# Kernel tuning notes

Measured on AMD Instinct MI355X. Metric: run time of the kernel, lower is better.

## Reference

```python
import jax, jax.numpy as jnp
import numpy as np
from itertools import product

_EPS = 1e-5
N_VOX = 120000
C = 64
B, D, H, Wd = 2, 400, 400, 40  # batch and spatial voxel grid


def _build_rulebook(seed=0):
    """Random unique active voxels + [N,27] submanifold neighbor index table (-1 = inactive)."""
    rng = np.random.default_rng(seed)
    size = B * D * H * Wd
    flat = rng.choice(size, size=N_VOX, replace=False)
    b = flat // (D * H * Wd)
    rem = flat % (D * H * Wd)
    z = rem // (H * Wd)
    rem2 = rem % (H * Wd)
    y = rem2 // Wd
    x = rem2 % Wd
    lut = np.full(size, -1, np.int32)
    lut[flat] = np.arange(N_VOX, dtype=np.int32)
    offs = np.array(list(product([-1, 0, 1], repeat=3)), dtype=np.int64)  # [27,3]
    zz = z[:, None] + offs[None, :, 0]
    yy = y[:, None] + offs[None, :, 1]
    xx = x[:, None] + offs[None, :, 2]
    valid = (zz >= 0) & (zz < D) & (yy >= 0) & (yy < H) & (xx >= 0) & (xx < Wd)
    nf = ((b[:, None] * D + zz) * H + yy) * Wd + xx
    nbr = np.where(valid, lut[np.clip(nf, 0, size - 1)], -1).astype(np.int32)
    return nbr


def setup_inputs() -> dict:
    key = jax.random.key(0)
    ks = jax.random.split(key, 12)
    nbr = jnp.asarray(_build_rulebook())
    return {
        "features": jax.random.normal(ks[0], (N_VOX, C), jnp.float32),
        "W1": jax.random.normal(ks[1], (27, C, C), jnp.float32) * 0.05,
        "g1": jax.random.uniform(ks[2], (C,), jnp.float32, 0.5, 1.5),
        "b1": jax.random.normal(ks[3], (C,), jnp.float32) * 0.1,
        "m1": jax.random.normal(ks[4], (C,), jnp.float32) * 0.1,
        "v1": jax.random.uniform(ks[5], (C,), jnp.float32, 0.5, 1.5),
        "W2": jax.random.normal(ks[6], (27, C, C), jnp.float32) * 0.05,
        "g2": jax.random.uniform(ks[7], (C,), jnp.float32, 0.5, 1.5),
        "b2": jax.random.normal(ks[8], (C,), jnp.float32) * 0.1,
        "m2": jax.random.normal(ks[9], (C,), jnp.float32) * 0.1,
        "v2": jax.random.uniform(ks[10], (C,), jnp.float32, 0.5, 1.5),
        "nbr_idx": nbr,
    }


def _subm_conv(f, nbr, W):
    # gather-GEMM: f [N,Cin], nbr [N,27], W [27,Cin,Cout] -> [N,Cout]
    mask = (nbr >= 0)[:, :, None]
    g = jnp.where(mask, f[jnp.clip(nbr, 0)], jnp.zeros((), f.dtype))  # [N,27,Cin]
    return jnp.einsum('nkc,kcd->nd', g, W)


def _bn(x, g, b, m, v):
    return (x - m) * (g * jax.lax.rsqrt(v + _EPS)) + b


def reference(features, W1, g1, b1, m1, v1, W2, g2, b2, m2, v2, nbr_idx):
    out = _bn(_subm_conv(features, nbr_idx, W1), g1, b1, m1, v1)
    out = jax.nn.relu(out)
    out = _bn(_subm_conv(out, nbr_idx, W2), g2, b2, m2, v2)
    return jax.nn.relu(out + features)
```

## Files before the change

kernel.cpp:

```cpp
#include <hip/hip_runtime.h>

typedef short short8 __attribute__((ext_vector_type(8)));
typedef float f32x4 __attribute__((ext_vector_type(4)));

#define N_VOX 120000
#define C64 64
#define K27 27
#define KC 13
#define TILES 3750
#define CAPT 64
#define LAYER_W 110592
#define CSRB 938
#define PACKB 65
#define FUSEB 938

#define WS_TCNT 0
#define WS_BNP  16384
#define WS_PWC  20480
#define WS_PWT  40960
#define WS_ENTS 524288
#define WS_MIDB (4u << 20)

__device__ __forceinline__ ushort f2bf(float x) {
    uint u = __float_as_uint(x);
    u = (u + 0x7FFFu + ((u >> 16) & 1u)) >> 16;
    return (ushort)u;
}
__device__ __forceinline__ float bf2f(ushort u) {
    return __uint_as_float((uint)u << 16);
}

__global__ __launch_bounds__(256) void prep_csr_kernel(
    const int* __restrict__ nbr,
    const float* __restrict__ W1, const float* __restrict__ W2,
    const float* g1, const float* b1, const float* m1, const float* v1,
    const float* g2, const float* b2, const float* m2, const float* v2,
    int* __restrict__ tcnt, int2* __restrict__ ents,
    ushort* __restrict__ pwt, ushort* __restrict__ pwc,
    float* __restrict__ bnp) {
    if (blockIdx.x < CSRB) {
        __shared__ int cnt_[4];
        const int wv = threadIdx.x >> 6, lane = threadIdx.x & 63;
        const int tile = blockIdx.x * 4 + wv;
        const bool act = tile < TILES;
        if (lane == 0) cnt_[wv] = 0;
        __syncthreads();
        if (act) {
            const int base = tile * (32 * K27);
            for (int e = lane; e < 32 * K27; e += 64) {
                const int k = e % K27;
                if (k == KC) continue;
                const int m = nbr[base + e];
                if (m >= 0) {
                    const int nl = e / K27;
                    int slot = atomicAdd(&cnt_[wv], 1);
                    if (slot < CAPT) ents[tile * CAPT + slot] = make_int2(nl | (k << 8), m);
                }
            }
        }
        __syncthreads();
        if (act && lane == 0) {
            int c = cnt_[wv];
            tcnt[tile] = c > CAPT ? CAPT : c;
        }
    } else {
        int idx = (blockIdx.x - CSRB) * 256 + threadIdx.x;
        const int stride = PACKB * 256;
        for (; idx < 229440; idx += stride) {
            if (idx < 221184) {
                int L = idx / LAYER_W, r = idx % LAYER_W;
                int k = r >> 12, dc = r & 4095, d = dc >> 6, c = dc & 63;
                const float* W = L ? W2 : W1;
                pwt[idx] = f2bf(W[(size_t)k * 4096 + c * 64 + d]);
            } else if (idx < 229376) {
                int j2 = idx - 221184;
                int L = j2 >> 12, q = j2 & 4095;
                int ks = q >> 11, tq = (q >> 9) & 3, ln = (q >> 3) & 63, jj = q & 7;
                int c = ks * 32 + (ln >> 4) * 8 + jj;
                int d = tq * 16 + (ln & 15);
                const float* W = L ? W2 : W1;
                pwc[L * 4096 + q] = f2bf(W[(size_t)KC * 4096 + c * 64 + d]);
            } else {
                int i = idx - 229376;
                float s1 = g1[i] * rsqrtf(v1[i] + 1e-5f);
                bnp[i] = s1; bnp[64 + i] = b1[i] - m1[i] * s1;
                float s2 = g2[i] * rsqrtf(v2[i] + 1e-5f);
                bnp[128 + i] = s2; bnp[192 + i] = b2[i] - m2[i] * s2;
            }
        }
    }
}

template <bool L2P>
__device__ __forceinline__ void fused_core(const float* __restrict__ f,
                                           const ushort* __restrict__ midin,
                                           const ushort* __restrict__ pwc,
                                           const ushort* __restrict__ pwt,
                                           const int* __restrict__ tcnt,
                                           const int2* __restrict__ ents,
                                           const float* __restrict__ bnp,
                                           ushort* __restrict__ midout,
                                           float* __restrict__ fout,
                                           float* exw, int tile) {
    const int lane = threadIdx.x & 63;
    const int r16 = lane & 15, kg = lane >> 4;
    const int n0 = tile * 32;

#pragma unroll
    for (int i = 0; i < 8; ++i) ((f32x4*)exw)[i * 64 + lane] = (f32x4)0.f;

    const short8* B = (const short8*)pwc;
    short8 Bf[2][4];
#pragma unroll
    for (int s = 0; s < 2; ++s)
#pragma unroll
        for (int t = 0; t < 4; ++t) Bf[s][t] = B[(s * 4 + t) * 64 + lane];

    f32x4 acc[2][4];
#pragma unroll
    for (int v = 0; v < 2; ++v)
#pragma unroll
        for (int t = 0; t < 4; ++t) acc[v][t] = (f32x4)0.f;

#pragma unroll
    for (int v = 0; v < 2; ++v) {
        short8 a0, a1;
        if (L2P) {
            const short8* ar = (const short8*)(midin + (size_t)(n0 + v * 16 + r16) * C64);
            a0 = ar[kg];
            a1 = ar[4 + kg];
        } else {
            const float4* ar = (const float4*)(f + (size_t)(n0 + v * 16 + r16) * C64);
            float4 fa = ar[kg * 2], fb = ar[kg * 2 + 1];
            float4 fc = ar[8 + kg * 2], fd = ar[9 + kg * 2];
            a0[0] = f2bf(fa.x); a0[1] = f2bf(fa.y); a0[2] = f2bf(fa.z); a0[3] = f2bf(fa.w);
            a0[4] = f2bf(fb.x); a0[5] = f2bf(fb.y); a0[6] = f2bf(fb.z); a0[7] = f2bf(fb.w);
            a1[0] = f2bf(fc.x); a1[1] = f2bf(fc.y); a1[2] = f2bf(fc.z); a1[3] = f2bf(fc.w);
            a1[4] = f2bf(fd.x); a1[5] = f2bf(fd.y); a1[6] = f2bf(fd.z); a1[7] = f2bf(fd.w);
        }
#pragma unroll
        for (int t = 0; t < 4; ++t) {
            acc[v][t] = __builtin_amdgcn_mfma_f32_16x16x32_bf16(a0, Bf[0][t], acc[v][t], 0, 0, 0);
            acc[v][t] = __builtin_amdgcn_mfma_f32_16x16x32_bf16(a1, Bf[1][t], acc[v][t], 0, 0, 0);
        }
    }

    const int cnt = tcnt[tile];
    for (int p = 0; p < cnt; ++p) {
        int2 e = ents[tile * CAPT + p];
        const int ex = __builtin_amdgcn_readfirstlane(e.x);
        const int m  = __builtin_amdgcn_readfirstlane(e.y);
        const int nl = ex & 255, k = ex >> 8;
        const short8* wr = (const short8*)(pwt + (size_t)k * 4096 + lane * 64);
        float ee0 = 0.f, ee1 = 0.f, ee2 = 0.f, ee3 = 0.f;
        if (L2P) {
            const uint* am = (const uint*)(midin + (size_t)m * C64);
#pragma unroll
            for (int g = 0; g < 8; ++g) {
                short8 w8 = wr[g];
                uint u0 = am[g * 4 + 0], u1 = am[g * 4 + 1];
                uint u2 = am[g * 4 + 2], u3 = am[g * 4 + 3];
                ee0 = fmaf(bf2f((ushort)u0),         bf2f((ushort)w8[0]), ee0);
                ee1 = fmaf(bf2f((ushort)(u0 >> 16)), bf2f((ushort)w8[1]), ee1);
                ee2 = fmaf(bf2f((ushort)u1),         bf2f((ushort)w8[2]), ee2);
                ee3 = fmaf(bf2f((ushort)(u1 >> 16)), bf2f((ushort)w8[3]), ee3);
                ee0 = fmaf(bf2f((ushort)u2),         bf2f((ushort)w8[4]), ee0);
                ee1 = fmaf(bf2f((ushort)(u2 >> 16)), bf2f((ushort)w8[5]), ee1);
                ee2 = fmaf(bf2f((ushort)u3),         bf2f((ushort)w8[6]), ee2);
                ee3 = fmaf(bf2f((ushort)(u3 >> 16)), bf2f((ushort)w8[7]), ee3);
            }
        } else {
            const float4* am = (const float4*)(f + (size_t)m * C64);
#pragma unroll
            for (int g = 0; g < 8; ++g) {
                short8 w8 = wr[g];
                float4 x0 = am[g * 2], x1 = am[g * 2 + 1];
                ee0 = fmaf(x0.x, bf2f((ushort)w8[0]), ee0);
                ee1 = fmaf(x0.y, bf2f((ushort)w8[1]), ee1);
                ee2 = fmaf(x0.z, bf2f((ushort)w8[2]), ee2);
                ee3 = fmaf(x0.w, bf2f((ushort)w8[3]), ee3);
                ee0 = fmaf(x1.x, bf2f((ushort)w8[4]), ee0);
                ee1 = fmaf(x1.y, bf2f((ushort)w8[5]), ee1);
                ee2 = fmaf(x1.z, bf2f((ushort)w8[6]), ee2);
                ee3 = fmaf(x1.w, bf2f((ushort)w8[7]), ee3);
            }
        }
        exw[nl * C64 + lane] += (ee0 + ee1) + (ee2 + ee3);
    }

#pragma unroll
    for (int v = 0; v < 2; ++v)
#pragma unroll
        for (int t = 0; t < 4; ++t)
#pragma unroll
            for (int r = 0; r < 4; ++r)
                exw[(v * 16 + kg * 4 + r) * C64 + t * 16 + r16] += acc[v][t][r];

    const int row = lane >> 1, col0 = (lane & 1) * 32;
    const f32x4* xl = (const f32x4*)(exw + row * C64 + col0);
    const size_t gbase = (size_t)(n0 + row) * C64 + col0;
    if (L2P) {
#pragma unroll
        for (int i = 0; i < 8; ++i) {
            f32x4 x = xl[i];
            float4 s  = *(const float4*)(bnp + col0 + i * 4);
            float4 h  = *(const float4*)(bnp + 64 + col0 + i * 4);
            float4 r4 = *(const float4*)(f + gbase + i * 4);
            float4 o;
            o.x = fmaxf(fmaf(x[0], s.x, h.x) + r4.x, 0.f);
            o.y = fmaxf(fmaf(x[1], s.y, h.y) + r4.y, 0.f);
            o.z = fmaxf(fmaf(x[2], s.z, h.z) + r4.z, 0.f);
            o.w = fmaxf(fmaf(x[3], s.w, h.w) + r4.w, 0.f);
            *(float4*)(fout + gbase + i * 4) = o;
        }
    } else {
#pragma unroll
        for (int i = 0; i < 4; ++i) {
            f32x4 x0 = xl[i * 2], x1 = xl[i * 2 + 1];
            float4 s0 = *(const float4*)(bnp + col0 + i * 8);
            float4 s1 = *(const float4*)(bnp + col0 + i * 8 + 4);
            float4 h0 = *(const float4*)(bnp + 64 + col0 + i * 8);
            float4 h1 = *(const float4*)(bnp + 64 + col0 + i * 8 + 4);
            short8 o;
            o[0] = f2bf(fmaxf(fmaf(x0[0], s0.x, h0.x), 0.f));
            o[1] = f2bf(fmaxf(fmaf(x0[1], s0.y, h0.y), 0.f));
            o[2] = f2bf(fmaxf(fmaf(x0[2], s0.z, h0.z), 0.f));
            o[3] = f2bf(fmaxf(fmaf(x0[3], s0.w, h0.w), 0.f));
            o[4] = f2bf(fmaxf(fmaf(x1[0], s1.x, h1.x), 0.f));
            o[5] = f2bf(fmaxf(fmaf(x1[1], s1.y, h1.y), 0.f));
            o[6] = f2bf(fmaxf(fmaf(x1[2], s1.z, h1.z), 0.f));
            o[7] = f2bf(fmaxf(fmaf(x1[3], s1.w, h1.w), 0.f));
            *(short8*)(midout + gbase + i * 8) = o;
        }
    }
}

__global__ __launch_bounds__(256) void fused_l1_kernel(const float* __restrict__ f,
                                                       const ushort* __restrict__ pwc,
                                                       const ushort* __restrict__ pwt,
                                                       const int* __restrict__ tcnt,
                                                       const int2* __restrict__ ents,
                                                       const float* __restrict__ bnp,
                                                       ushort* __restrict__ midb) {
    __shared__ float ext[4][32 * C64];
    const int wv = threadIdx.x >> 6;
    const int tile = blockIdx.x * 4 + wv;
    if (tile >= TILES) return;
    fused_core<false>(f, nullptr, pwc, pwt, tcnt, ents, bnp, midb, nullptr, ext[wv], tile);
}

__global__ __launch_bounds__(256) void fused_l2_kernel(const float* __restrict__ f,
                                                       const ushort* __restrict__ midb,
                                                       const ushort* __restrict__ pwc,
                                                       const ushort* __restrict__ pwt,
                                                       const int* __restrict__ tcnt,
                                                       const int2* __restrict__ ents,
                                                       const float* __restrict__ bnp,
                                                       float* __restrict__ out) {
    __shared__ float ext[4][32 * C64];
    const int wv = threadIdx.x >> 6;
    const int tile = blockIdx.x * 4 + wv;
    if (tile >= TILES) return;
    fused_core<true>(f, midb, pwc, pwt, tcnt, ents, bnp, nullptr, out, ext[wv], tile);
}

extern "C" void kernel_launch(void* const* d_in, const int* in_sizes, int n_in,
                              void* d_out, int out_size, void* d_ws, size_t ws_size,
                              hipStream_t stream) {
    const float* f   = (const float*)d_in[0];
    const float* W1  = (const float*)d_in[1];
    const float* g1  = (const float*)d_in[2];
    const float* b1  = (const float*)d_in[3];
    const float* m1  = (const float*)d_in[4];
    const float* v1  = (const float*)d_in[5];
    const float* W2  = (const float*)d_in[6];
    const float* g2  = (const float*)d_in[7];
    const float* b2  = (const float*)d_in[8];
    const float* m2  = (const float*)d_in[9];
    const float* v2  = (const float*)d_in[10];
    const int*   nbr = (const int*)d_in[11];
    float* out = (float*)d_out;

    char* ws = (char*)d_ws;
    int*    tcnt = (int*)(ws + WS_TCNT);
    float*  bnp  = (float*)(ws + WS_BNP);
    ushort* pwc  = (ushort*)(ws + WS_PWC);
    ushort* pwt  = (ushort*)(ws + WS_PWT);
    int2*   ents = (int2*)(ws + WS_ENTS);
    ushort* midb = (ushort*)(ws + WS_MIDB);

    prep_csr_kernel<<<CSRB + PACKB, 256, 0, stream>>>(
        nbr, W1, W2, g1, b1, m1, v1, g2, b2, m2, v2, tcnt, ents, pwt, pwc, bnp);

    fused_l1_kernel<<<FUSEB, 256, 0, stream>>>(f, pwc, pwt, tcnt, ents, bnp, midb);
    fused_l2_kernel<<<FUSEB, 256, 0, stream>>>(f, midb, pwc + 4096, pwt + LAYER_W,
                                               tcnt, ents, bnp + 128, out);
}
```

Baseline: 205.4 us.

## Shrink voxel tiles to 16 rows and stage neighbor entries in LDS

Halves the per-wave tile from 32 to 16 voxels, doubling the number of waves so more of them are resident, and cuts per-wave LDS use. The tile's neighbor-entry list is copied once into shared memory, and the pair loop is unrolled by two. LDS rows get padding to avoid bank conflicts, and the weight-pack stage becomes one element per thread. The trade-off is a smaller centre-tap MFMA per wave and a lower CAPT of 48, which raises the chance of silently dropping neighbor pairs in dense tiles.

```diff
diff --git a/kernel.cpp b/kernel.cpp
--- a/kernel.cpp
+++ b/kernel.cpp
@@ -7,17 +7,18 @@
 #define C64 64
 #define K27 27
 #define KC 13
-#define TILES 3750
-#define CAPT 64
+#define TIL 7500
+#define CAPT 48
+#define PAD 68
 #define LAYER_W 110592
-#define CSRB 938
-#define PACKB 65
-#define FUSEB 938
+#define CSRB 1875
+#define PACKB 897
+#define FUSEB 1875
 
 #define WS_TCNT 0
-#define WS_BNP  16384
-#define WS_PWC  20480
-#define WS_PWT  40960
+#define WS_BNP  32768
+#define WS_PWC  36864
+#define WS_PWT  65536
 #define WS_ENTS 524288
 #define WS_MIDB (4u << 20)
 
@@ -42,53 +43,93 @@
         __shared__ int cnt_[4];
         const int wv = threadIdx.x >> 6, lane = threadIdx.x & 63;
         const int tile = blockIdx.x * 4 + wv;
-        const bool act = tile < TILES;
         if (lane == 0) cnt_[wv] = 0;
         __syncthreads();
-        if (act) {
-            const int base = tile * (32 * K27);
-            for (int e = lane; e < 32 * K27; e += 64) {
-                const int k = e % K27;
-                if (k == KC) continue;
-                const int m = nbr[base + e];
-                if (m >= 0) {
-                    const int nl = e / K27;
-                    int slot = atomicAdd(&cnt_[wv], 1);
-                    if (slot < CAPT) ents[tile * CAPT + slot] = make_int2(nl | (k << 8), m);
-                }
+        const int base = tile * (16 * K27);
+#pragma unroll
+        for (int e = lane; e < 16 * K27; e += 64) {
+            const int k = e % K27;
+            if (k == KC) continue;
+            const int m = nbr[base + e];
+            if (m >= 0) {
+                const int nl = e / K27;
+                int slot = atomicAdd(&cnt_[wv], 1);
+                if (slot < CAPT) ents[tile * CAPT + slot] = make_int2(nl | (k << 8), m);
             }
         }
         __syncthreads();
-        if (act && lane == 0) {
+        if (lane == 0) {
             int c = cnt_[wv];
             tcnt[tile] = c > CAPT ? CAPT : c;
         }
     } else {
-        int idx = (blockIdx.x - CSRB) * 256 + threadIdx.x;
-        const int stride = PACKB * 256;
-        for (; idx < 229440; idx += stride) {
-            if (idx < 221184) {
-                int L = idx / LAYER_W, r = idx % LAYER_W;
-                int k = r >> 12, dc = r & 4095, d = dc >> 6, c = dc & 63;
-                const float* W = L ? W2 : W1;
-                pwt[idx] = f2bf(W[(size_t)k * 4096 + c * 64 + d]);
-            } else if (idx < 229376) {
-                int j2 = idx - 221184;
-                int L = j2 >> 12, q = j2 & 4095;
-                int ks = q >> 11, tq = (q >> 9) & 3, ln = (q >> 3) & 63, jj = q & 7;
-                int c = ks * 32 + (ln >> 4) * 8 + jj;
-                int d = tq * 16 + (ln & 15);
-                const float* W = L ? W2 : W1;
-                pwc[L * 4096 + q] = f2bf(W[(size_t)KC * 4096 + c * 64 + d]);
-            } else {
-                int i = idx - 229376;
-                float s1 = g1[i] * rsqrtf(v1[i] + 1e-5f);
-                bnp[i] = s1; bnp[64 + i] = b1[i] - m1[i] * s1;
-                float s2 = g2[i] * rsqrtf(v2[i] + 1e-5f);
-                bnp[128 + i] = s2; bnp[192 + i] = b2[i] - m2[i] * s2;
-            }
-        }
-    }
+        const int idx = (blockIdx.x - CSRB) * 256 + threadIdx.x;
+        if (idx < 221184) {
+            int L = idx / LAYER_W, r = idx % LAYER_W;
+            int k = r >> 12, dc = r & 4095, d = dc >> 6, c = dc & 63;
+            const float* W = L ? W2 : W1;
+            pwt[idx] = f2bf(W[(size_t)k * 4096 + c * 64 + d]);
+        } else if (idx < 229376) {
+            int j2 = idx - 221184;
+            int L = j2 >> 12, q = j2 & 4095;
+            int ks = q >> 11, tq = (q >> 9) & 3, ln = (q >> 3) & 63, jj = q & 7;
+            int c = ks * 32 + (ln >> 4) * 8 + jj;
+            int d = tq * 16 + (ln & 15);
+            const float* W = L ? W2 : W1;
+            pwc[L * 4096 + q] = f2bf(W[(size_t)KC * 4096 + c * 64 + d]);
+        } else if (idx < 229440) {
+            int i = idx - 229376;
+            float s1 = g1[i] * rsqrtf(v1[i] + 1e-5f);
+            bnp[i] = s1; bnp[64 + i] = b1[i] - m1[i] * s1;
+            float s2 = g2[i] * rsqrtf(v2[i] + 1e-5f);
+            bnp[128 + i] = s2; bnp[192 + i] = b2[i] - m2[i] * s2;
+        }
+    }
+}
+
+template <bool L2P>
+__device__ __forceinline__ void pair_body(const float* __restrict__ f,
+                                          const ushort* __restrict__ midin,
+                                          const ushort* __restrict__ pwt,
+                                          int2 e, int lane, float* exw) {
+    const int ex = __builtin_amdgcn_readfirstlane(e.x);
+    const int m  = __builtin_amdgcn_readfirstlane(e.y);
+    const int nl = ex & 255, k = ex >> 8;
+    const short8* wr = (const short8*)(pwt + (size_t)k * 4096 + lane * 64);
+    float ee0 = 0.f, ee1 = 0.f, ee2 = 0.f, ee3 = 0.f;
+    if (L2P) {
+        const uint* am = (const uint*)(midin + (size_t)m * C64);
+#pragma unroll
+        for (int g = 0; g < 8; ++g) {
+            short8 w8 = wr[g];
+            uint u0 = am[g * 4 + 0], u1 = am[g * 4 + 1];
+            uint u2 = am[g * 4 + 2], u3 = am[g * 4 + 3];
+            ee0 = fmaf(bf2f((ushort)u0),         bf2f((ushort)w8[0]), ee0);
+            ee1 = fmaf(bf2f((ushort)(u0 >> 16)), bf2f((ushort)w8[1]), ee1);
+            ee2 = fmaf(bf2f((ushort)u1),         bf2f((ushort)w8[2]), ee2);
+            ee3 = fmaf(bf2f((ushort)(u1 >> 16)), bf2f((ushort)w8[3]), ee3);
+            ee0 = fmaf(bf2f((ushort)u2),         bf2f((ushort)w8[4]), ee0);
+            ee1 = fmaf(bf2f((ushort)(u2 >> 16)), bf2f((ushort)w8[5]), ee1);
+            ee2 = fmaf(bf2f((ushort)u3),         bf2f((ushort)w8[6]), ee2);
+            ee3 = fmaf(bf2f((ushort)(u3 >> 16)), bf2f((ushort)w8[7]), ee3);
+        }
+    } else {
+        const float4* am = (const float4*)(f + (size_t)m * C64);
+#pragma unroll
+        for (int g = 0; g < 8; ++g) {
+            short8 w8 = wr[g];
+            float4 x0 = am[g * 2], x1 = am[g * 2 + 1];
+            ee0 = fmaf(x0.x, bf2f((ushort)w8[0]), ee0);
+            ee1 = fmaf(x0.y, bf2f((ushort)w8[1]), ee1);
+            ee2 = fmaf(x0.z, bf2f((ushort)w8[2]), ee2);
+            ee3 = fmaf(x0.w, bf2f((ushort)w8[3]), ee3);
+            ee0 = fmaf(x1.x, bf2f((ushort)w8[4]), ee0);
+            ee1 = fmaf(x1.y, bf2f((ushort)w8[5]), ee1);
+            ee2 = fmaf(x1.z, bf2f((ushort)w8[6]), ee2);
+            ee3 = fmaf(x1.w, bf2f((ushort)w8[7]), ee3);
+        }
+    }
+    exw[nl * PAD + lane] += (ee0 + ee1) + (ee2 + ee3);
 }
 
 template <bool L2P>
@@ -101,13 +142,20 @@
                                            const float* __restrict__ bnp,
                                            ushort* __restrict__ midout,
                                            float* __restrict__ fout,
-                                           float* exw, int tile) {
+                                           float* exw, int2* sents, int tile) {
     const int lane = threadIdx.x & 63;
     const int r16 = lane & 15, kg = lane >> 4;
-    const int n0 = tile * 32;
-
-#pragma unroll
-    for (int i = 0; i < 8; ++i) ((f32x4*)exw)[i * 64 + lane] = (f32x4)0.f;
+    const int n0 = tile * 16;
+
+    const int cnt = tcnt[tile];
+    if (lane < cnt) sents[lane] = ents[(size_t)tile * CAPT + lane];
+
+    {
+        const int zr = lane >> 2, zc = (lane & 3) * 16;
+        f32x4* zp = (f32x4*)(exw + zr * PAD + zc);
+#pragma unroll
+        for (int i = 0; i < 4; ++i) zp[i] = (f32x4)0.f;
+    }
 
     const short8* B = (const short8*)pwc;
     short8 Bf[2][4];
@@ -116,92 +164,50 @@
 #pragma unroll
         for (int t = 0; t < 4; ++t) Bf[s][t] = B[(s * 4 + t) * 64 + lane];
 
-    f32x4 acc[2][4];
-#pragma unroll
-    for (int v = 0; v < 2; ++v)
-#pragma unroll
-        for (int t = 0; t < 4; ++t) acc[v][t] = (f32x4)0.f;
-
-#pragma unroll
-    for (int v = 0; v < 2; ++v) {
-        short8 a0, a1;
-        if (L2P) {
-            const short8* ar = (const short8*)(midin + (size_t)(n0 + v * 16 + r16) * C64);
-            a0 = ar[kg];
-            a1 = ar[4 + kg];
-        } else {
-            const float4* ar = (const float4*)(f + (size_t)(n0 + v * 16 + r16) * C64);
-            float4 fa = ar[kg * 2], fb = ar[kg * 2 + 1];
-            float4 fc = ar[8 + kg * 2], fd = ar[9 + kg * 2];
-            a0[0] = f2bf(fa.x); a0[1] = f2bf(fa.y); a0[2] = f2bf(fa.z); a0[3] = f2bf(fa.w);
-            a0[4] = f2bf(fb.x); a0[5] = f2bf(fb.y); a0[6] = f2bf(fb.z); a0[7] = f2bf(fb.w);
-            a1[0] = f2bf(fc.x); a1[1] = f2bf(fc.y); a1[2] = f2bf(fc.z); a1[3] = f2bf(fc.w);
-            a1[4] = f2bf(fd.x); a1[5] = f2bf(fd.y); a1[6] = f2bf(fd.z); a1[7] = f2bf(fd.w);
-        }
-#pragma unroll
-        for (int t = 0; t < 4; ++t) {
-            acc[v][t] = __builtin_amdgcn_mfma_f32_16x16x32_bf16(a0, Bf[0][t], acc[v][t], 0, 0, 0);
-            acc[v][t] = __builtin_amdgcn_mfma_f32_16x16x32_bf16(a1, Bf[1][t], acc[v][t], 0, 0, 0);
-        }
-    }
-
-    const int cnt = tcnt[tile];
-    for (int p = 0; p < cnt; ++p) {
-        int2 e = ents[tile * CAPT + p];
-        const int ex = __builtin_amdgcn_readfirstlane(e.x);
-        const int m  = __builtin_amdgcn_readfirstlane(e.y);
-        const int nl = ex & 255, k = ex >> 8;
-        const short8* wr = (const short8*)(pwt + (size_t)k * 4096 + lane * 64);
-        float ee0 = 0.f, ee1 = 0.f, ee2 = 0.f, ee3 = 0.f;
-        if (L2P) {
-            const uint* am = (const uint*)(midin + (size_t)m * C64);
-#pragma unroll
-            for (int g = 0; g < 8; ++g) {
-                short8 w8 = wr[g];
-                uint u0 = am[g * 4 + 0], u1 = am[g * 4 + 1];
-                uint u2 = am[g * 4 + 2], u3 = am[g * 4 + 3];
-                ee0 = fmaf(bf2f((ushort)u0),         bf2f((ushort)w8[0]), ee0);
-                ee1 = fmaf(bf2f((ushort)(u0 >> 16)), bf2f((ushort)w8[1]), ee1);
-                ee2 = fmaf(bf2f((ushort)u1),         bf2f((ushort)w8[2]), ee2);
-                ee3 = fmaf(bf2f((ushort)(u1 >> 16)), bf2f((ushort)w8[3]), ee3);
-                ee0 = fmaf(bf2f((ushort)u2),         bf2f((ushort)w8[4]), ee0);
-                ee1 = fmaf(bf2f((ushort)(u2 >> 16)), bf2f((ushort)w8[5]), ee1);
-                ee2 = fmaf(bf2f((ushort)u3),         bf2f((ushort)w8[6]), ee2);
-                ee3 = fmaf(bf2f((ushort)(u3 >> 16)), bf2f((ushort)w8[7]), ee3);
-            }
-        } else {
-            const float4* am = (const float4*)(f + (size_t)m * C64);
-#pragma unroll
-            for (int g = 0; g < 8; ++g) {
-                short8 w8 = wr[g];
-                float4 x0 = am[g * 2], x1 = am[g * 2 + 1];
-                ee0 = fmaf(x0.x, bf2f((ushort)w8[0]), ee0);
-                ee1 = fmaf(x0.y, bf2f((ushort)w8[1]), ee1);
-                ee2 = fmaf(x0.z, bf2f((ushort)w8[2]), ee2);
-                ee3 = fmaf(x0.w, bf2f((ushort)w8[3]), ee3);
-                ee0 = fmaf(x1.x, bf2f((ushort)w8[4]), ee0);
-                ee1 = fmaf(x1.y, bf2f((ushort)w8[5]), ee1);
-                ee2 = fmaf(x1.z, bf2f((ushort)w8[6]), ee2);
-                ee3 = fmaf(x1.w, bf2f((ushort)w8[7]), ee3);
-            }
-        }
-        exw[nl * C64 + lane] += (ee0 + ee1) + (ee2 + ee3);
-    }
-
-#pragma unroll
-    for (int v = 0; v < 2; ++v)
-#pragma unroll
-        for (int t = 0; t < 4; ++t)
-#pragma unroll
-            for (int r = 0; r < 4; ++r)
-                exw[(v * 16 + kg * 4 + r) * C64 + t * 16 + r16] += acc[v][t][r];
-
-    const int row = lane >> 1, col0 = (lane & 1) * 32;
-    const f32x4* xl = (const f32x4*)(exw + row * C64 + col0);
+    short8 a0, a1;
+    if (L2P) {
+        const short8* ar = (const short8*)(midin + (size_t)(n0 + r16) * C64);
+        a0 = ar[kg];
+        a1 = ar[4 + kg];
+    } else {
+        const float4* ar = (const float4*)(f + (size_t)(n0 + r16) * C64);
+        float4 fa = ar[kg * 2], fb = ar[kg * 2 + 1];
+        float4 fc = ar[8 + kg * 2], fd = ar[9 + kg * 2];
+        a0[0] = f2bf(fa.x); a0[1] = f2bf(fa.y); a0[2] = f2bf(fa.z); a0[3] = f2bf(fa.w);
+        a0[4] = f2bf(fb.x); a0[5] = f2bf(fb.y); a0[6] = f2bf(fb.z); a0[7] = f2bf(fb.w);
+        a1[0] = f2bf(fc.x); a1[1] = f2bf(fc.y); a1[2] = f2bf(fc.z); a1[3] = f2bf(fc.w);
+        a1[4] = f2bf(fd.x); a1[5] = f2bf(fd.y); a1[6] = f2bf(fd.z); a1[7] = f2bf(fd.w);
+    }
+
+    f32x4 acc[4];
+#pragma unroll
+    for (int t = 0; t < 4; ++t) acc[t] = (f32x4)0.f;
+#pragma unroll
+    for (int t = 0; t < 4; ++t) {
+        acc[t] = __builtin_amdgcn_mfma_f32_16x16x32_bf16(a0, Bf[0][t], acc[t], 0, 0, 0);
+        acc[t] = __builtin_amdgcn_mfma_f32_16x16x32_bf16(a1, Bf[1][t], acc[t], 0, 0, 0);
+    }
+
+    int p = 0;
+    for (; p + 1 < cnt; p += 2) {
+        int2 e0 = sents[p], e1 = sents[p + 1];
+        pair_body<L2P>(f, midin, pwt, e0, lane, exw);
+        pair_body<L2P>(f, midin, pwt, e1, lane, exw);
+    }
+    if (p < cnt) pair_body<L2P>(f, midin, pwt, sents[p], lane, exw);
+
+#pragma unroll
+    for (int t = 0; t < 4; ++t)
+#pragma unroll
+        for (int r = 0; r < 4; ++r)
+            exw[(kg * 4 + r) * PAD + t * 16 + r16] += acc[t][r];
+
+    const int row = lane >> 2, col0 = (lane & 3) * 16;
+    const f32x4* xl = (const f32x4*)(exw + row * PAD + col0);
     const size_t gbase = (size_t)(n0 + row) * C64 + col0;
     if (L2P) {
 #pragma unroll
-        for (int i = 0; i < 8; ++i) {
+        for (int i = 0; i < 4; ++i) {
             f32x4 x = xl[i];
             float4 s  = *(const float4*)(bnp + col0 + i * 4);
             float4 h  = *(const float4*)(bnp + 64 + col0 + i * 4);
@@ -215,7 +221,7 @@
         }
     } else {
 #pragma unroll
-        for (int i = 0; i < 4; ++i) {
+        for (int i = 0; i < 2; ++i) {
             f32x4 x0 = xl[i * 2], x1 = xl[i * 2 + 1];
             float4 s0 = *(const float4*)(bnp + col0 + i * 8);
             float4 s1 = *(const float4*)(bnp + col0 + i * 8 + 4);
@@ -242,11 +248,12 @@
                                                        const int2* __restrict__ ents,
                                                        const float* __restrict__ bnp,
                                                        ushort* __restrict__ midb) {
-    __shared__ float ext[4][32 * C64];
+    __shared__ float ext[4][16 * PAD];
+    __shared__ int2  sents[4][CAPT];
     const int wv = threadIdx.x >> 6;
     const int tile = blockIdx.x * 4 + wv;
-    if (tile >= TILES) return;
-    fused_core<false>(f, nullptr, pwc, pwt, tcnt, ents, bnp, midb, nullptr, ext[wv], tile);
+    fused_core<false>(f, nullptr, pwc, pwt, tcnt, ents, bnp, midb, nullptr,
+                      ext[wv], sents[wv], tile);
 }
 
 __global__ __launch_bounds__(256) void fused_l2_kernel(const float* __restrict__ f,
@@ -257,11 +264,12 @@
                                                        const int2* __restrict__ ents,
                                                        const float* __restrict__ bnp,
                                                        float* __restrict__ out) {
-    __shared__ float ext[4][32 * C64];
+    __shared__ float ext[4][16 * PAD];
+    __shared__ int2  sents[4][CAPT];
     const int wv = threadIdx.x >> 6;
     const int tile = blockIdx.x * 4 + wv;
-    if (tile >= TILES) return;
-    fused_core<true>(f, midb, pwc, pwt, tcnt, ents, bnp, nullptr, out, ext[wv], tile);
+    fused_core<true>(f, midb, pwc, pwt, tcnt, ents, bnp, nullptr, out,
+                     ext[wv], sents[wv], tile);
 }
 
 extern "C" void kernel_launch(void* const* d_in, const int* in_sizes, int n_in,
```

Result: slower. 213.7 us (+4.0%).

## Process neighbor entries in pairs, stage rulebook in LDS, one-wave blocks

Applied to the files above, without the earlier changes.

The neighbor-entry loop now handles two rulebook entries per iteration with independent accumulators, so two gathers and weight-row loads can be in flight at once. A tile's entries are staged in shared memory before the loop. The shared scratch tile is padded to a row stride of 66 floats to spread accesses across LDS banks. Fused kernels launch one 64-thread block per tile, and the weight pack stage uses one thread per element instead of a strided loop, at the cost of more blocks and extra register pressure from the paired loop.

```diff
diff --git a/kernel.cpp b/kernel.cpp
--- a/kernel.cpp
+++ b/kernel.cpp
@@ -9,10 +9,10 @@
 #define KC 13
 #define TILES 3750
 #define CAPT 64
+#define PAD 66
 #define LAYER_W 110592
 #define CSRB 938
-#define PACKB 65
-#define FUSEB 938
+#define PACKB 897
 
 #define WS_TCNT 0
 #define WS_BNP  16384
@@ -64,31 +64,145 @@
             tcnt[tile] = c > CAPT ? CAPT : c;
         }
     } else {
-        int idx = (blockIdx.x - CSRB) * 256 + threadIdx.x;
-        const int stride = PACKB * 256;
-        for (; idx < 229440; idx += stride) {
-            if (idx < 221184) {
-                int L = idx / LAYER_W, r = idx % LAYER_W;
-                int k = r >> 12, dc = r & 4095, d = dc >> 6, c = dc & 63;
-                const float* W = L ? W2 : W1;
-                pwt[idx] = f2bf(W[(size_t)k * 4096 + c * 64 + d]);
-            } else if (idx < 229376) {
-                int j2 = idx - 221184;
-                int L = j2 >> 12, q = j2 & 4095;
-                int ks = q >> 11, tq = (q >> 9) & 3, ln = (q >> 3) & 63, jj = q & 7;
-                int c = ks * 32 + (ln >> 4) * 8 + jj;
-                int d = tq * 16 + (ln & 15);
-                const float* W = L ? W2 : W1;
-                pwc[L * 4096 + q] = f2bf(W[(size_t)KC * 4096 + c * 64 + d]);
-            } else {
-                int i = idx - 229376;
-                float s1 = g1[i] * rsqrtf(v1[i] + 1e-5f);
-                bnp[i] = s1; bnp[64 + i] = b1[i] - m1[i] * s1;
-                float s2 = g2[i] * rsqrtf(v2[i] + 1e-5f);
-                bnp[128 + i] = s2; bnp[192 + i] = b2[i] - m2[i] * s2;
-            }
-        }
-    }
+        const int idx = (blockIdx.x - CSRB) * 256 + threadIdx.x;
+        if (idx < 221184) {
+            int L = idx / LAYER_W, r = idx % LAYER_W;
+            int k = r >> 12, dc = r & 4095, d = dc >> 6, c = dc & 63;
+            const float* W = L ? W2 : W1;
+            pwt[idx] = f2bf(W[(size_t)k * 4096 + c * 64 + d]);
+        } else if (idx < 229376) {
+            int j2 = idx - 221184;
+            int L = j2 >> 12, q = j2 & 4095;
+            int ks = q >> 11, tq = (q >> 9) & 3, ln = (q >> 3) & 63, jj = q & 7;
+            int c = ks * 32 + (ln >> 4) * 8 + jj;
+            int d = tq * 16 + (ln & 15);
+            const float* W = L ? W2 : W1;
+            pwc[L * 4096 + q] = f2bf(W[(size_t)KC * 4096 + c * 64 + d]);
+        } else if (idx < 229440) {
+            int i = idx - 229376;
+            float s1 = g1[i] * rsqrtf(v1[i] + 1e-5f);
+            bnp[i] = s1; bnp[64 + i] = b1[i] - m1[i] * s1;
+            float s2 = g2[i] * rsqrtf(v2[i] + 1e-5f);
+            bnp[128 + i] = s2; bnp[192 + i] = b2[i] - m2[i] * s2;
+        }
+    }
+}
+
+template <bool L2P>
+__device__ __forceinline__ void pair2_body(const float* __restrict__ f,
+                                           const ushort* __restrict__ midin,
+                                           const ushort* __restrict__ pwt,
+                                           int2 e0, int2 e1, int lane, float* exw) {
+    const int ex0 = __builtin_amdgcn_readfirstlane(e0.x);
+    const int m0  = __builtin_amdgcn_readfirstlane(e0.y);
+    const int ex1 = __builtin_amdgcn_readfirstlane(e1.x);
+    const int m1  = __builtin_amdgcn_readfirstlane(e1.y);
+    const int nl0 = ex0 & 255, k0 = ex0 >> 8;
+    const int nl1 = ex1 & 255, k1 = ex1 >> 8;
+    const short8* wra = (const short8*)(pwt + (size_t)k0 * 4096 + lane * 64);
+    const short8* wrb = (const short8*)(pwt + (size_t)k1 * 4096 + lane * 64);
+    float a0 = 0.f, a1 = 0.f, a2 = 0.f, a3 = 0.f;
+    float b0 = 0.f, b1 = 0.f, b2 = 0.f, b3 = 0.f;
+    if (L2P) {
+        const uint* ama = (const uint*)(midin + (size_t)m0 * C64);
+        const uint* amb = (const uint*)(midin + (size_t)m1 * C64);
+#pragma unroll
+        for (int g = 0; g < 8; ++g) {
+            short8 wa = wra[g], wb = wrb[g];
+            uint ua0 = ama[g * 4 + 0], ua1 = ama[g * 4 + 1];
+            uint ua2 = ama[g * 4 + 2], ua3 = ama[g * 4 + 3];
+            uint ub0 = amb[g * 4 + 0], ub1 = amb[g * 4 + 1];
+            uint ub2 = amb[g * 4 + 2], ub3 = amb[g * 4 + 3];
+            a0 = fmaf(bf2f((ushort)ua0),         bf2f((ushort)wa[0]), a0);
+            a1 = fmaf(bf2f((ushort)(ua0 >> 16)), bf2f((ushort)wa[1]), a1);
+            a2 = fmaf(bf2f((ushort)ua1),         bf2f((ushort)wa[2]), a2);
+            a3 = fmaf(bf2f((ushort)(ua1 >> 16)), bf2f((ushort)wa[3]), a3);
+            b0 = fmaf(bf2f((ushort)ub0),         bf2f((ushort)wb[0]), b0);
+            b1 = fmaf(bf2f((ushort)(ub0 >> 16)), bf2f((ushort)wb[1]), b1);
+            b2 = fmaf(bf2f((ushort)ub1),         bf2f((ushort)wb[2]), b2);
+            b3 = fmaf(bf2f((ushort)(ub1 >> 16)), bf2f((ushort)wb[3]), b3);
+            a0 = fmaf(bf2f((ushort)ua2),         bf2f((ushort)wa[4]), a0);
+            a1 = fmaf(bf2f((ushort)(ua2 >> 16)), bf2f((ushort)wa[5]), a1);
+            a2 = fmaf(bf2f((ushort)ua3),         bf2f((ushort)wa[6]), a2);
+            a3 = fmaf(bf2f((ushort)(ua3 >> 16)), bf2f((ushort)wa[7]), a3);
+            b0 = fmaf(bf2f((ushort)ub2),         bf2f((ushort)wb[4]), b0);
+            b1 = fmaf(bf2f((ushort)(ub2 >> 16)), bf2f((ushort)wb[5]), b1);
+            b2 = fmaf(bf2f((ushort)ub3),         bf2f((ushort)wb[6]), b2);
+            b3 = fmaf(bf2f((ushort)(ub3 >> 16)), bf2f((ushort)wb[7]), b3);
+        }
+    } else {
+        const float4* ama = (const float4*)(f + (size_t)m0 * C64);
+        const float4* amb = (const float4*)(f + (size_t)m1 * C64);
+#pragma unroll
+        for (int g = 0; g < 8; ++g) {
+            short8 wa = wra[g], wb = wrb[g];
+            float4 xa0 = ama[g * 2], xa1 = ama[g * 2 + 1];
+            float4 xb0 = amb[g * 2], xb1 = amb[g * 2 + 1];
+            a0 = fmaf(xa0.x, bf2f((ushort)wa[0]), a0);
+            a1 = fmaf(xa0.y, bf2f((ushort)wa[1]), a1);
+            a2 = fmaf(xa0.z, bf2f((ushort)wa[2]), a2);
+            a3 = fmaf(xa0.w, bf2f((ushort)wa[3]), a3);
+            b0 = fmaf(xb0.x, bf2f((ushort)wb[0]), b0);
+            b1 = fmaf(xb0.y, bf2f((ushort)wb[1]), b1);
+            b2 = fmaf(xb0.z, bf2f((ushort)wb[2]), b2);
+            b3 = fmaf(xb0.w, bf2f((ushort)wb[3]), b3);
+            a0 = fmaf(xa1.x, bf2f((ushort)wa[4]), a0);
+            a1 = fmaf(xa1.y, bf2f((ushort)wa[5]), a1);
+            a2 = fmaf(xa1.z, bf2f((ushort)wa[6]), a2);
+            a3 = fmaf(xa1.w, bf2f((ushort)wa[7]), a3);
+            b0 = fmaf(xb1.x, bf2f((ushort)wb[4]), b0);
+            b1 = fmaf(xb1.y, bf2f((ushort)wb[5]), b1);
+            b2 = fmaf(xb1.z, bf2f((ushort)wb[6]), b2);
+            b3 = fmaf(xb1.w, bf2f((ushort)wb[7]), b3);
+        }
+    }
+    exw[nl0 * PAD + lane] += (a0 + a1) + (a2 + a3);
+    exw[nl1 * PAD + lane] += (b0 + b1) + (b2 + b3);
+}
+
+template <bool L2P>
+__device__ __forceinline__ void pair1_body(const float* __restrict__ f,
+                                           const ushort* __restrict__ midin,
+                                           const ushort* __restrict__ pwt,
+                                           int2 e, int lane, float* exw) {
+    const int ex = __builtin_amdgcn_readfirstlane(e.x);
+    const int m  = __builtin_amdgcn_readfirstlane(e.y);
+    const int nl = ex & 255, k = ex >> 8;
+    const short8* wr = (const short8*)(pwt + (size_t)k * 4096 + lane * 64);
+    float a0 = 0.f, a1 = 0.f, a2 = 0.f, a3 = 0.f;
+    if (L2P) {
+        const uint* am = (const uint*)(midin + (size_t)m * C64);
+#pragma unroll
+        for (int g = 0; g < 8; ++g) {
+            short8 w8 = wr[g];
+            uint u0 = am[g * 4 + 0], u1 = am[g * 4 + 1];
+            uint u2 = am[g * 4 + 2], u3 = am[g * 4 + 3];
+            a0 = fmaf(bf2f((ushort)u0),         bf2f((ushort)w8[0]), a0);
+            a1 = fmaf(bf2f((ushort)(u0 >> 16)), bf2f((ushort)w8[1]), a1);
+            a2 = fmaf(bf2f((ushort)u1),         bf2f((ushort)w8[2]), a2);
+            a3 = fmaf(bf2f((ushort)(u1 >> 16)), bf2f((ushort)w8[3]), a3);
+            a0 = fmaf(bf2f((ushort)u2),         bf2f((ushort)w8[4]), a0);
+            a1 = fmaf(bf2f((ushort)(u2 >> 16)), bf2f((ushort)w8[5]), a1);
+            a2 = fmaf(bf2f((ushort)u3),         bf2f((ushort)w8[6]), a2);
+            a3 = fmaf(bf2f((ushort)(u3 >> 16)), bf2f((ushort)w8[7]), a3);
+        }
+    } else {
+        const float4* am = (const float4*)(f + (size_t)m * C64);
+#pragma unroll
+        for (int g = 0; g < 8; ++g) {
+            short8 w8 = wr[g];
+            float4 x0 = am[g * 2], x1 = am[g * 2 + 1];
+            a0 = fmaf(x0.x, bf2f((ushort)w8[0]), a0);
+            a1 = fmaf(x0.y, bf2f((ushort)w8[1]), a1);
+            a2 = fmaf(x0.z, bf2f((ushort)w8[2]), a2);
+            a3 = fmaf(x0.w, bf2f((ushort)w8[3]), a3);
+            a0 = fmaf(x1.x, bf2f((ushort)w8[4]), a0);
+            a1 = fmaf(x1.y, bf2f((ushort)w8[5]), a1);
+            a2 = fmaf(x1.z, bf2f((ushort)w8[6]), a2);
+            a3 = fmaf(x1.w, bf2f((ushort)w8[7]), a3);
+        }
+    }
+    exw[nl * PAD + lane] += (a0 + a1) + (a2 + a3);
 }
 
 template <bool L2P>
@@ -101,13 +215,20 @@
                                            const float* __restrict__ bnp,
                                            ushort* __restrict__ midout,
                                            float* __restrict__ fout,
-                                           float* exw, int tile) {
+                                           float* exw, int2* sents, int tile) {
     const int lane = threadIdx.x & 63;
     const int r16 = lane & 15, kg = lane >> 4;
     const int n0 = tile * 32;
 
-#pragma unroll
-    for (int i = 0; i < 8; ++i) ((f32x4*)exw)[i * 64 + lane] = (f32x4)0.f;
+    const int cnt = tcnt[tile];
+    if (lane < cnt) sents[lane] = ents[(size_t)tile * CAPT + lane];
+
+    {
+        const int zr = lane >> 1, zc = (lane & 1) * 32;
+        f32x4* zp = (f32x4*)(exw + zr * PAD + zc);
+#pragma unroll
+        for (int i = 0; i < 8; ++i) zp[i] = (f32x4)0.f;
+    }
 
     const short8* B = (const short8*)pwc;
     short8 Bf[2][4];
@@ -145,48 +266,11 @@
         }
     }
 
-    const int cnt = tcnt[tile];
-    for (int p = 0; p < cnt; ++p) {
-        int2 e = ents[tile * CAPT + p];
-        const int ex = __builtin_amdgcn_readfirstlane(e.x);
-        const int m  = __builtin_amdgcn_readfirstlane(e.y);
-        const int nl = ex & 255, k = ex >> 8;
-        const short8* wr = (const short8*)(pwt + (size_t)k * 4096 + lane * 64);
-        float ee0 = 0.f, ee1 = 0.f, ee2 = 0.f, ee3 = 0.f;
-        if (L2P) {
-            const uint* am = (const uint*)(midin + (size_t)m * C64);
-#pragma unroll
-            for (int g = 0; g < 8; ++g) {
-                short8 w8 = wr[g];
-                uint u0 = am[g * 4 + 0], u1 = am[g * 4 + 1];
-                uint u2 = am[g * 4 + 2], u3 = am[g * 4 + 3];
-                ee0 = fmaf(bf2f((ushort)u0),         bf2f((ushort)w8[0]), ee0);
-                ee1 = fmaf(bf2f((ushort)(u0 >> 16)), bf2f((ushort)w8[1]), ee1);
-                ee2 = fmaf(bf2f((ushort)u1),         bf2f((ushort)w8[2]), ee2);
-                ee3 = fmaf(bf2f((ushort)(u1 >> 16)), bf2f((ushort)w8[3]), ee3);
-                ee0 = fmaf(bf2f((ushort)u2),         bf2f((ushort)w8[4]), ee0);
-                ee1 = fmaf(bf2f((ushort)(u2 >> 16)), bf2f((ushort)w8[5]), ee1);
-                ee2 = fmaf(bf2f((ushort)u3),         bf2f((ushort)w8[6]), ee2);
-                ee3 = fmaf(bf2f((ushort)(u3 >> 16)), bf2f((ushort)w8[7]), ee3);
-            }
-        } else {
-            const float4* am = (const float4*)(f + (size_t)m * C64);
-#pragma unroll
-            for (int g = 0; g < 8; ++g) {
-                short8 w8 = wr[g];
-                float4 x0 = am[g * 2], x1 = am[g * 2 + 1];
-                ee0 = fmaf(x0.x, bf2f((ushort)w8[0]), ee0);
-                ee1 = fmaf(x0.y, bf2f((ushort)w8[1]), ee1);
-                ee2 = fmaf(x0.z, bf2f((ushort)w8[2]), ee2);
-                ee3 = fmaf(x0.w, bf2f((ushort)w8[3]), ee3);
-                ee0 = fmaf(x1.x, bf2f((ushort)w8[4]), ee0);
-                ee1 = fmaf(x1.y, bf2f((ushort)w8[5]), ee1);
-                ee2 = fmaf(x1.z, bf2f((ushort)w8[6]), ee2);
-                ee3 = fmaf(x1.w, bf2f((ushort)w8[7]), ee3);
-            }
-        }
-        exw[nl * C64 + lane] += (ee0 + ee1) + (ee2 + ee3);
-    }
+    int p = 0;
+    for (; p + 1 < cnt; p += 2)
+        pair2_body<L2P>(f, midin, pwt, sents[p], sents[p + 1], lane, exw);
+    if (p < cnt)
+        pair1_body<L2P>(f, midin, pwt, sents[p], lane, exw);
 
 #pragma unroll
     for (int v = 0; v < 2; ++v)
@@ -194,10 +278,10 @@
         for (int t = 0; t < 4; ++t)
 #pragma unroll
             for (int r = 0; r < 4; ++r)
-                exw[(v * 16 + kg * 4 + r) * C64 + t * 16 + r16] += acc[v][t][r];
+                exw[(v * 16 + kg * 4 + r) * PAD + t * 16 + r16] += acc[v][t][r];
 
     const int row = lane >> 1, col0 = (lane & 1) * 32;
-    const f32x4* xl = (const f32x4*)(exw + row * C64 + col0);
+    const f32x4* xl = (const f32x4*)(exw + row * PAD + col0);
     const size_t gbase = (size_t)(n0 + row) * C64 + col0;
     if (L2P) {
 #pragma unroll
@@ -235,33 +319,31 @@
     }
 }
 
-__global__ __launch_bounds__(256) void fused_l1_kernel(const float* __restrict__ f,
-                                                       const ushort* __restrict__ pwc,
-                                                       const ushort* __restrict__ pwt,
-                                                       const int* __restrict__ tcnt,
-                                                       const int2* __restrict__ ents,
-                                                       const float* __restrict__ bnp,
-                                                       ushort* __restrict__ midb) {
-    __shared__ float ext[4][32 * C64];
-    const int wv = threadIdx.x >> 6;
-    const int tile = blockIdx.x * 4 + wv;
-    if (tile >= TILES) return;
-    fused_core<false>(f, nullptr, pwc, pwt, tcnt, ents, bnp, midb, nullptr, ext[wv], tile);
-}
-
-__global__ __launch_bounds__(256) void fused_l2_kernel(const float* __restrict__ f,
-                                                       const ushort* __restrict__ midb,
-                                                       const ushort* __restrict__ pwc,
-                                                       const ushort* __restrict__ pwt,
-                                                       const int* __restrict__ tcnt,
-                                                       const int2* __restrict__ ents,
-                                                       const float* __restrict__ bnp,
-                                                       float* __restrict__ out) {
-    __shared__ float ext[4][32 * C64];
-    const int wv = threadIdx.x >> 6;
-    const int tile = blockIdx.x * 4 + wv;
-    if (tile >= TILES) return;
-    fused_core<true>(f, midb, pwc, pwt, tcnt, ents, bnp, nullptr, out, ext[wv], tile);
+__global__ __launch_bounds__(64) void fused_l1_kernel(const float* __restrict__ f,
+                                                      const ushort* __restrict__ pwc,
+                                                      const ushort* __restrict__ pwt,
+                                                      const int* __restrict__ tcnt,
+                                                      const int2* __restrict__ ents,
+                                                      const float* __restrict__ bnp,
+                                                      ushort* __restrict__ midb) {
+    __shared__ float ext[32 * PAD];
+    __shared__ int2  sents[CAPT];
+    fused_core<false>(f, nullptr, pwc, pwt, tcnt, ents, bnp, midb, nullptr,
+                      ext, sents, blockIdx.x);
+}
+
+__global__ __launch_bounds__(64) void fused_l2_kernel(const float* __restrict__ f,
+                                                      const ushort* __restrict__ midb,
+                                                      const ushort* __restrict__ pwc,
+                                                      const ushort* __restrict__ pwt,
+                                                      const int* __restrict__ tcnt,
+                                                      const int2* __restrict__ ents,
+                                                      const float* __restrict__ bnp,
+                                                      float* __restrict__ out) {
+    __shared__ float ext[32 * PAD];
+    __shared__ int2  sents[CAPT];
+    fused_core<true>(f, midb, pwc, pwt, tcnt, ents, bnp, nullptr, out,
+                     ext, sents, blockIdx.x);
 }
 
 extern "C" void kernel_launch(void* const* d_in, const int* in_sizes, int n_in,
@@ -292,7 +374,7 @@
     prep_csr_kernel<<<CSRB + PACKB, 256, 0, stream>>>(
         nbr, W1, W2, g1, b1, m1, v1, g2, b2, m2, v2, tcnt, ents, pwt, pwc, bnp);
 
-    fused_l1_kernel<<<FUSEB, 256, 0, stream>>>(f, pwc, pwt, tcnt, ents, bnp, midb);
-    fused_l2_kernel<<<FUSEB, 256, 0, stream>>>(f, midb, pwc + 4096, pwt + LAYER_W,
-                                               tcnt, ents, bnp + 128, out);
-}
+    fused_l1_kernel<<<TILES, 64, 0, stream>>>(f, pwc, pwt, tcnt, ents, bnp, midb);
+    fused_l2_kernel<<<TILES, 64, 0, stream>>>(f, midb, pwc + 4096, pwt + LAYER_W,
+                                              tcnt, ents, bnp + 128, out);
+}
```

After: 232.2 us. +13.0%, slower.
